# Performance work log

Hardware: AMD Instinct MI355X
Metric: run time of the kernel (lower is better)

Reference implementation:

```python
import math
import jax, jax.numpy as jnp
import numpy as np


def _proj(x, w, b):
    # 1x1x1 Conv3d == pointwise channel matmul: (B,C,T,H,W) x (O,C) -> (B,O,T,H,W)
    return jnp.einsum('bcthw,oc->bothw', x, w) + b[None, :, None, None, None]


def setup_inputs() -> dict:
    key = jax.random.key(0)
    ks = jax.random.split(key, 16)
    B, C, T, H, W = 2, 64, 16, 14, 14
    CI = C // 2
    s_in = 1.0 / math.sqrt(C)
    s_out = 1.0 / math.sqrt(CI)
    inp = {'x': jax.random.normal(ks[0], (B, C, T, H, W), jnp.float32)}
    # QKV projections for spatial (s) and temporal (t) branches: (CI, C) weights
    pnames = ['qs', 'ks', 'vs', 'qt', 'kt', 'vt']
    for i, n in enumerate(pnames):
        inp['W' + n] = jax.random.normal(ks[1 + i], (CI, C), jnp.float32) * s_in
        inp['b' + n] = jax.random.normal(ks[7 + i], (CI,), jnp.float32) * 0.01
    # output projection W: (C, CI)
    inp['Ww'] = jax.random.normal(ks[13], (C, CI), jnp.float32) * s_out
    inp['bw'] = jax.random.normal(ks[14], (C,), jnp.float32) * 0.01
    return inp


def reference(x, Wqs, bqs, Wks, bks, Wvs, bvs, Wqt, bqt, Wkt, bkt, Wvt, bvt, Ww, bw):
    B, C, T, H, W = x.shape
    CI = Wqs.shape[0]
    N = CI * H * W  # flat dim after original's raw .view (mixes channel & spatial/time)
    scale = 1.0 / math.sqrt(T)

    # ---- spatial branch: .view(B, T, -1) raw reshape of (B,CI,T,H,W) ----
    qs = _proj(x, Wqs, bqs).reshape(B, T, N).transpose(0, 2, 1)   # (B,N,T)
    ks_ = _proj(x, Wks, bks).reshape(B, T, N)                     # (B,T,N)
    vs = _proj(x, Wvs, bvs).reshape(B, T, N).transpose(0, 2, 1)   # (B,N,T)
    attn_s = jax.nn.softmax(jnp.einsum('bnt,btm->bnm', qs, ks_) * scale, axis=-1)  # (B,N,N)
    ys = jnp.einsum('bnm,bmt->bnt', attn_s, vs)                   # (B,N,T)
    ys = ys.transpose(0, 2, 1).reshape(B, CI, T, H, W)

    # ---- temporal branch: .view(B, CI*H*W, -1) raw reshape ----
    qt = _proj(x, Wqt, bqt).reshape(B, N, T).transpose(0, 2, 1)   # (B,T,N)
    kt = _proj(x, Wkt, bkt).reshape(B, N, T)                      # (B,N,T)
    vt = _proj(x, Wvt, bvt).reshape(B, N, T).transpose(0, 2, 1)   # (B,T,N)
    attn_t = jax.nn.softmax(jnp.einsum('btn,bns->bts', qt, kt) * scale, axis=-1)  # (B,T,T)
    yt = jnp.einsum('bts,bsn->btn', attn_t, vt)                   # (B,T,N)
    yt = yt.transpose(0, 2, 1).reshape(B, CI, T, H, W)

    y = ys + yt
    return _proj(y, Ww, bw) + x
```

## Files before the change

### kernel.cpp

```cpp
#include <hip/hip_runtime.h>
#include <math.h>

#define S3   3136
#define PB   100352
#define XB   200704
#define NN   6272
#define MW   7
#define MPW  896
#define TGC  49

typedef __attribute__((ext_vector_type(8))) short bf16x8;
typedef __attribute__((ext_vector_type(4))) float f32x4;

__device__ inline ushort f2bf(float f) {
    uint u = __float_as_uint(f);
    return (ushort)((u + 0x7FFFu + ((u >> 16) & 1u)) >> 16);
}

__global__ __launch_bounds__(256) void proj_kernel(
    const float* __restrict__ x,
    const float* __restrict__ W0, const float* __restrict__ b0,
    const float* __restrict__ W1, const float* __restrict__ b1,
    const float* __restrict__ W2, const float* __restrict__ b2,
    const float* __restrict__ W3, const float* __restrict__ b3,
    const float* __restrict__ W4, const float* __restrict__ b4,
    const float* __restrict__ W5, const float* __restrict__ b5,
    ushort* __restrict__ Qb, ushort* __restrict__ Kb, ushort* __restrict__ Vb,
    float* __restrict__ Qt, float* __restrict__ Kt, float* __restrict__ Vt)
{
    const float* Wp; const float* bp;
    switch (blockIdx.y) {
        case 0:  Wp = W0; bp = b0; break;
        case 1:  Wp = W1; bp = b1; break;
        case 2:  Wp = W2; bp = b2; break;
        case 3:  Wp = W3; bp = b3; break;
        case 4:  Wp = W4; bp = b4; break;
        default: Wp = W5; bp = b5; break;
    }
    int z = blockIdx.z;

    int gid = blockIdx.x * 256 + threadIdx.x;
    if (gid >= 2 * S3) return;
    int b = (gid >= S3) ? 1 : 0;
    int s = gid - b * S3;

    float xr[64];
    #pragma unroll
    for (int c = 0; c < 64; ++c) xr[c] = x[(size_t)b * XB + (size_t)c * S3 + s];

    float a[16];
    #pragma unroll
    for (int oo = 0; oo < 16; ++oo) {
        int o = z * 16 + oo;
        float acc = bp[o];
        #pragma unroll
        for (int c = 0; c < 64; ++c) acc = fmaf(Wp[o * 64 + c], xr[c], acc);
        a[oo] = acc;
    }

    if (blockIdx.y < 2) {
        const float sc = (blockIdx.y == 0) ? 0.36067376022224085f : 1.0f;
        ushort* ob = (blockIdx.y == 0) ? Qb : Kb;
        #pragma unroll
        for (int h = 0; h < 2; ++h) {
            int n = h * S3 + s;
            uint u0 = f2bf(a[0 + h] * sc)  | ((uint)f2bf(a[2 + h]  * sc) << 16);
            uint u1 = f2bf(a[4 + h] * sc)  | ((uint)f2bf(a[6 + h]  * sc) << 16);
            uint u2 = f2bf(a[8 + h] * sc)  | ((uint)f2bf(a[10 + h] * sc) << 16);
            uint u3 = f2bf(a[12 + h] * sc) | ((uint)f2bf(a[14 + h] * sc) << 16);
            *(uint4*)(ob + ((size_t)(b * NN + n) * 16 + z * 8)) = make_uint4(u0, u1, u2, u3);
        }
    } else if (blockIdx.y == 2) {
        #pragma unroll
        for (int oo = 0; oo < 16; ++oo) {
            int o = z * 16 + oo;
            Vb[(size_t)(b * 16 + (o >> 1)) * NN + (o & 1) * S3 + s] = f2bf(a[oo]);
        }
    } else {
        float* op = (blockIdx.y == 3) ? Qt : (blockIdx.y == 4) ? Kt : Vt;
        #pragma unroll
        for (int oo = 0; oo < 16; ++oo)
            op[(size_t)b * PB + (size_t)(z * 16 + oo) * S3 + s] = a[oo];
    }
}

__global__ __launch_bounds__(256) void attn_kernel(
    const ushort* __restrict__ Qb, const ushort* __restrict__ Kb,
    const ushort* __restrict__ Vb, const float* __restrict__ Qt,
    const float* __restrict__ Kt,
    float* __restrict__ Pacc, float* __restrict__ Pl, float* __restrict__ Gp)
{
    __shared__ ushort ptile[4][16 * 40];
    __shared__ float qs[128 * 16], ks[128 * 16];

    int b = blockIdx.y;

    if (blockIdx.x >= 686) {
        int c = blockIdx.x - 686;
        size_t base = (size_t)b * PB + (size_t)c * 2048;
        for (int i = threadIdx.x; i < 512; i += 256) {
            ((float4*)qs)[i] = ((const float4*)(Qt + base))[i];
            ((float4*)ks)[i] = ((const float4*)(Kt + base))[i];
        }
        __syncthreads();
        int t = threadIdx.x >> 4, s = threadIdx.x & 15;
        float acc = 0.0f;
        #pragma unroll 8
        for (int n = 0; n < 128; ++n)
            acc = fmaf(qs[n * 16 + t], ks[n * 16 + s], acc);
        Gp[(size_t)(b * TGC + c) * 256 + threadIdx.x] = acc;
        return;
    }

    int wave = __builtin_amdgcn_readfirstlane((int)(threadIdx.x >> 6));
    int lane = threadIdx.x & 63;
    int col  = lane & 15;
    int kg   = lane >> 4;
    int gw   = blockIdx.x * 4 + wave;
    int ntile = gw / 7;
    int w     = gw - ntile * 7;
    int nbase = ntile * 16;
    int m0    = w * MPW;

    bf16x8 qf = {0, 0, 0, 0, 0, 0, 0, 0};
    if (kg < 2)
        qf = *(const bf16x8*)(Qb + ((size_t)(b * NN + nbase + col) * 16 + kg * 8));

    const bf16x8 ones = {16256, 16256, 16256, 16256, 16256, 16256, 16256, 16256};
    f32x4 zero4 = {0.f, 0.f, 0.f, 0.f};
    f32x4 yacc  = zero4;
    f32x4 lacc  = zero4;

    ushort* myt = ptile[wave];

    for (int it = 0; it < MPW / 32; ++it) {
        int mb = m0 + it * 32;
        bf16x8 vf = *(const bf16x8*)(Vb + ((size_t)(b * 16 + col) * NN + mb + kg * 8));

        #pragma unroll
        for (int tile = 0; tile < 2; ++tile) {
            int mt = mb + tile * 16;
            bf16x8 kf = {0, 0, 0, 0, 0, 0, 0, 0};
            if (kg < 2)
                kf = *(const bf16x8*)(Kb + ((size_t)(b * NN + mt + col) * 16 + kg * 8));
            f32x4 st = __builtin_amdgcn_mfma_f32_16x16x32_bf16(kf, qf, zero4, 0, 0, 0);
            float p0 = __builtin_amdgcn_exp2f(st[0]);
            float p1 = __builtin_amdgcn_exp2f(st[1]);
            float p2 = __builtin_amdgcn_exp2f(st[2]);
            float p3 = __builtin_amdgcn_exp2f(st[3]);
            uint lo = f2bf(p0) | ((uint)f2bf(p1) << 16);
            uint hi = f2bf(p2) | ((uint)f2bf(p3) << 16);
            *(uint2*)(myt + (col * 40 + tile * 16 + kg * 4)) = make_uint2(lo, hi);
        }
        bf16x8 pf = *(bf16x8*)(myt + (col * 40 + kg * 8));
        yacc = __builtin_amdgcn_mfma_f32_16x16x32_bf16(vf, pf, yacc, 0, 0, 0);
        lacc = __builtin_amdgcn_mfma_f32_16x16x32_bf16(ones, pf, lacc, 0, 0, 0);
    }

    #pragma unroll
    for (int r = 0; r < 4; ++r) {
        int t = kg * 4 + r;
        Pacc[((size_t)(b * 16 + t) * MW + w) * NN + nbase + col] = yacc[r];
    }
    if (kg == 0)
        Pl[((size_t)b * MW + w) * NN + nbase + col] = lacc[0];
}

__global__ __launch_bounds__(256) void merge_final(
    const float* __restrict__ Pacc, const float* __restrict__ Pl,
    const float* __restrict__ Gp, const float* __restrict__ Vt,
    const float* __restrict__ x, const float* __restrict__ Ww,
    const float* __restrict__ bw, float* __restrict__ out)
{
    __shared__ float Lsh[256];
    __shared__ float Ash[16][17];
    __shared__ float Wsh[64 * 36];
    __shared__ float Ysh[16 * 36];

    int b  = blockIdx.y;
    int sc = blockIdx.x;

    {
        float a = 0.0f;
        for (int c = 0; c < TGC; ++c)
            a += Gp[(size_t)(b * TGC + c) * 256 + threadIdx.x];
        Lsh[threadIdx.x] = a * 0.25f;
        for (int i = threadIdx.x; i < 2048; i += 256)
            Wsh[(i >> 5) * 36 + (i & 31)] = Ww[i];
    }
    __syncthreads();
    if (threadIdx.x < 16) {
        int t = threadIdx.x;
        const float* Lr = &Lsh[t * 16];
        float mx = -1e30f;
        #pragma unroll
        for (int s = 0; s < 16; ++s) mx = fmaxf(mx, Lr[s]);
        float e[16]; float sm = 0.0f;
        #pragma unroll
        for (int s = 0; s < 16; ++s) { e[s] = __expf(Lr[s] - mx); sm += e[s]; }
        float inv = 1.0f / sm;
        #pragma unroll
        for (int s = 0; s < 16; ++s) Ash[s][t] = e[s] * inv;
    }
    __syncthreads();

    #pragma unroll
    for (int k = 0; k < 2; ++k) {
        int idx = threadIdx.x + k * 256;
        int ss = idx & 15;
        int ci = idx >> 4;
        int s  = sc * 16 + ss;
        int t  = ci >> 1;
        int nn = (ci & 1) * S3 + s;

        float a = 0.0f, l = 0.0f;
        #pragma unroll
        for (int w = 0; w < MW; ++w) {
            a += Pacc[((size_t)(b * 16 + t) * MW + w) * NN + nn];
            l += Pl[((size_t)b * MW + w) * NN + nn];
        }
        float ys = a / l;

        int t2 = nn & 15;
        const float4* vp = (const float4*)(Vt + (size_t)b * PB + (size_t)t * NN + (nn & ~15));
        float4 v0 = vp[0], v1 = vp[1], v2 = vp[2], v3 = vp[3];
        float yt = Ash[0][t2] * v0.x;
        yt = fmaf(Ash[1][t2],  v0.y, yt); yt = fmaf(Ash[2][t2],  v0.z, yt);
        yt = fmaf(Ash[3][t2],  v0.w, yt); yt = fmaf(Ash[4][t2],  v1.x, yt);
        yt = fmaf(Ash[5][t2],  v1.y, yt); yt = fmaf(Ash[6][t2],  v1.z, yt);
        yt = fmaf(Ash[7][t2],  v1.w, yt); yt = fmaf(Ash[8][t2],  v2.x, yt);
        yt = fmaf(Ash[9][t2],  v2.y, yt); yt = fmaf(Ash[10][t2], v2.z, yt);
        yt = fmaf(Ash[11][t2], v2.w, yt); yt = fmaf(Ash[12][t2], v3.x, yt);
        yt = fmaf(Ash[13][t2], v3.y, yt); yt = fmaf(Ash[14][t2], v3.z, yt);
        yt = fmaf(Ash[15][t2], v3.w, yt);

        Ysh[ss * 36 + ci] = ys + yt;
    }
    __syncthreads();

    int ss = threadIdx.x & 15;
    int cg = threadIdx.x >> 4;
    int s  = sc * 16 + ss;

    float acc[4];
    #pragma unroll
    for (int k = 0; k < 4; ++k) acc[k] = bw[cg * 4 + k];

    #pragma unroll
    for (int cb = 0; cb < 32; cb += 4) {
        float4 y4 = *(const float4*)&Ysh[ss * 36 + cb];
        #pragma unroll
        for (int k = 0; k < 4; ++k) {
            float4 w4 = *(const float4*)&Wsh[(cg * 4 + k) * 36 + cb];
            acc[k] = fmaf(w4.x, y4.x, acc[k]);
            acc[k] = fmaf(w4.y, y4.y, acc[k]);
            acc[k] = fmaf(w4.z, y4.z, acc[k]);
            acc[k] = fmaf(w4.w, y4.w, acc[k]);
        }
    }

    #pragma unroll
    for (int k = 0; k < 4; ++k) {
        int c = cg * 4 + k;
        size_t o = (size_t)b * XB + (size_t)c * S3 + s;
        out[o] = x[o] + acc[k];
    }
}

extern "C" void kernel_launch(void* const* d_in, const int* in_sizes, int n_in,
                              void* d_out, int out_size, void* d_ws, size_t ws_size,
                              hipStream_t stream)
{
    const float* x   = (const float*)d_in[0];
    const float* Wqs = (const float*)d_in[1];  const float* bqs = (const float*)d_in[2];
    const float* Wks = (const float*)d_in[3];  const float* bks = (const float*)d_in[4];
    const float* Wvs = (const float*)d_in[5];  const float* bvs = (const float*)d_in[6];
    const float* Wqt = (const float*)d_in[7];  const float* bqt = (const float*)d_in[8];
    const float* Wkt = (const float*)d_in[9];  const float* bkt = (const float*)d_in[10];
    const float* Wvt = (const float*)d_in[11]; const float* bvt = (const float*)d_in[12];
    const float* Ww  = (const float*)d_in[13]; const float* bw  = (const float*)d_in[14];

    float* ws = (float*)d_ws;
    ushort* Qb = (ushort*)(ws);
    ushort* Kb = (ushort*)(ws + 100352);
    ushort* Vb = (ushort*)(ws + 200704);
    float* Qt  = ws + 301056;
    float* Kt  = ws + 501760;
    float* Vt  = ws + 702464;
    float* Gp  = ws + 903168;
    float* Pacc = ws + 928256;
    float* Pl   = ws + 2333184;

    proj_kernel<<<dim3(25, 6, 2), 256, 0, stream>>>(
        x, Wqs, bqs, Wks, bks, Wvs, bvs, Wqt, bqt, Wkt, bkt, Wvt, bvt,
        Qb, Kb, Vb, Qt, Kt, Vt);

    attn_kernel<<<dim3(686 + TGC, 2), 256, 0, stream>>>(
        Qb, Kb, Vb, Qt, Kt, Pacc, Pl, Gp);

    merge_final<<<dim3(196, 2), 256, 0, stream>>>(
        Pacc, Pl, Gp, Vt, x, Ww, bw, (float*)d_out);
}
```

Baseline: 142.1 us.

## Fuse three kernels into one persistent kernel with grid barriers

Merges the projection, attention and merge/output kernels into one persistent launch of 512 blocks that separates the stages with software grid barriers built on atomic counters. A memset resets the counters before each launch. The projection loop now loads x in chunks of 16 channels to lower register pressure, and the attention work is spread over the waves in a grid-stride loop. This removes two kernel launch gaps, but adds barrier spin costs, a memset launch, and depends on all 512 blocks being resident at once.

```diff
diff --git a/kernel.cpp b/kernel.cpp
--- a/kernel.cpp
+++ b/kernel.cpp
@@ -8,6 +8,8 @@
 #define MW   7
 #define MPW  896
 #define TGC  49
+#define GRID 512
+#define SPB  464
 
 typedef __attribute__((ext_vector_type(8))) short bf16x8;
 typedef __attribute__((ext_vector_type(4))) float f32x4;
@@ -17,253 +19,273 @@
     return (ushort)((u + 0x7FFFu + ((u >> 16) & 1u)) >> 16);
 }
 
-__global__ __launch_bounds__(256) void proj_kernel(
-    const float* __restrict__ x,
-    const float* __restrict__ W0, const float* __restrict__ b0,
-    const float* __restrict__ W1, const float* __restrict__ b1,
-    const float* __restrict__ W2, const float* __restrict__ b2,
-    const float* __restrict__ W3, const float* __restrict__ b3,
-    const float* __restrict__ W4, const float* __restrict__ b4,
-    const float* __restrict__ W5, const float* __restrict__ b5,
-    ushort* __restrict__ Qb, ushort* __restrict__ Kb, ushort* __restrict__ Vb,
-    float* __restrict__ Qt, float* __restrict__ Kt, float* __restrict__ Vt)
+__device__ inline void grid_barrier(int* ctr, int nblk) {
+    __syncthreads();
+    if (threadIdx.x == 0) {
+        __threadfence();
+        atomicAdd(ctr, 1);
+        while (__hip_atomic_load(ctr, __ATOMIC_RELAXED,
+                                 __HIP_MEMORY_SCOPE_AGENT) < nblk)
+            __builtin_amdgcn_s_sleep(8);
+        __threadfence();
+    }
+    __syncthreads();
+}
+
+struct Params {
+    const float *x;
+    const float *W[6];
+    const float *bias[6];
+    const float *Ww, *bw;
+    int    *bar;
+    ushort *Qb, *Kb, *Vb;
+    float  *Qt, *Kt, *Vt;
+    float  *Gp, *Pacc, *Pl;
+    float  *out;
+};
+
+__global__ __launch_bounds__(256, 4) void fused_kernel(Params p)
 {
-    const float* Wp; const float* bp;
-    switch (blockIdx.y) {
-        case 0:  Wp = W0; bp = b0; break;
-        case 1:  Wp = W1; bp = b1; break;
-        case 2:  Wp = W2; bp = b2; break;
-        case 3:  Wp = W3; bp = b3; break;
-        case 4:  Wp = W4; bp = b4; break;
-        default: Wp = W5; bp = b5; break;
-    }
-    int z = blockIdx.z;
-
-    int gid = blockIdx.x * 256 + threadIdx.x;
-    if (gid >= 2 * S3) return;
-    int b = (gid >= S3) ? 1 : 0;
-    int s = gid - b * S3;
-
-    float xr[64];
-    #pragma unroll
-    for (int c = 0; c < 64; ++c) xr[c] = x[(size_t)b * XB + (size_t)c * S3 + s];
-
-    float a[16];
-    #pragma unroll
-    for (int oo = 0; oo < 16; ++oo) {
-        int o = z * 16 + oo;
-        float acc = bp[o];
+    __shared__ __align__(16) char smem[16384];
+    const int tid = threadIdx.x;
+    const int bid = blockIdx.x;
+
+    {
+        int gid = bid * 256 + tid;
+        if (gid < 75264) {
+            int bs = gid % 6272;
+            int yz = gid / 6272;
+            int y = yz >> 1, z = yz & 1;
+            int b = (bs >= S3) ? 1 : 0;
+            int s = bs - b * S3;
+
+            const float* Wp = p.W[y];
+            const float* bp = p.bias[y];
+
+            float a[16];
+            #pragma unroll
+            for (int oo = 0; oo < 16; ++oo) a[oo] = bp[z * 16 + oo];
+
+            #pragma unroll
+            for (int cc = 0; cc < 4; ++cc) {
+                float xr[16];
+                #pragma unroll
+                for (int k = 0; k < 16; ++k)
+                    xr[k] = p.x[(size_t)b * XB + (size_t)(cc * 16 + k) * S3 + s];
+                #pragma unroll
+                for (int oo = 0; oo < 16; ++oo) {
+                    int o = z * 16 + oo;
+                    #pragma unroll
+                    for (int k = 0; k < 16; ++k)
+                        a[oo] = fmaf(Wp[o * 64 + cc * 16 + k], xr[k], a[oo]);
+                }
+            }
+
+            if (y < 2) {
+                const float sc = (y == 0) ? 0.36067376022224085f : 1.0f;
+                ushort* ob = (y == 0) ? p.Qb : p.Kb;
+                #pragma unroll
+                for (int h = 0; h < 2; ++h) {
+                    int n = h * S3 + s;
+                    uint u0 = f2bf(a[0 + h] * sc)  | ((uint)f2bf(a[2 + h]  * sc) << 16);
+                    uint u1 = f2bf(a[4 + h] * sc)  | ((uint)f2bf(a[6 + h]  * sc) << 16);
+                    uint u2 = f2bf(a[8 + h] * sc)  | ((uint)f2bf(a[10 + h] * sc) << 16);
+                    uint u3 = f2bf(a[12 + h] * sc) | ((uint)f2bf(a[14 + h] * sc) << 16);
+                    *(uint4*)(ob + ((size_t)(b * NN + n) * 16 + z * 8)) =
+                        make_uint4(u0, u1, u2, u3);
+                }
+            } else if (y == 2) {
+                #pragma unroll
+                for (int oo = 0; oo < 16; ++oo) {
+                    int o = z * 16 + oo;
+                    p.Vb[(size_t)(b * 16 + (o >> 1)) * NN + (o & 1) * S3 + s] = f2bf(a[oo]);
+                }
+            } else {
+                float* op = (y == 3) ? p.Qt : (y == 4) ? p.Kt : p.Vt;
+                #pragma unroll
+                for (int oo = 0; oo < 16; ++oo)
+                    op[(size_t)b * PB + (size_t)(z * 16 + oo) * S3 + s] = a[oo];
+            }
+        }
+    }
+
+    grid_barrier(p.bar + 0, GRID);
+
+    if (bid < SPB) {
+        int wave = __builtin_amdgcn_readfirstlane((int)(tid >> 6));
+        int lane = tid & 63;
+        int col  = lane & 15;
+        int kg   = lane >> 4;
+        int gwave = bid * 4 + wave;
+        ushort* myt = (ushort*)(smem + wave * 1280);
+        const bf16x8 ones = {16256, 16256, 16256, 16256, 16256, 16256, 16256, 16256};
+        f32x4 zero4 = {0.f, 0.f, 0.f, 0.f};
+
+        for (int task = gwave; task < 2 * 2744; task += SPB * 4) {
+            int b = task / 2744;
+            int r = task - b * 2744;
+            int ntile = r / 7;
+            int w     = r - ntile * 7;
+            int nbase = ntile * 16;
+            int m0    = w * MPW;
+
+            bf16x8 qf = {0, 0, 0, 0, 0, 0, 0, 0};
+            if (kg < 2)
+                qf = *(const bf16x8*)(p.Qb + ((size_t)(b * NN + nbase + col) * 16 + kg * 8));
+
+            f32x4 yacc = zero4;
+            f32x4 lacc = zero4;
+
+            for (int it = 0; it < MPW / 32; ++it) {
+                int mb = m0 + it * 32;
+                bf16x8 vf = *(const bf16x8*)(p.Vb + ((size_t)(b * 16 + col) * NN + mb + kg * 8));
+
+                #pragma unroll
+                for (int tile = 0; tile < 2; ++tile) {
+                    int mt = mb + tile * 16;
+                    bf16x8 kf = {0, 0, 0, 0, 0, 0, 0, 0};
+                    if (kg < 2)
+                        kf = *(const bf16x8*)(p.Kb + ((size_t)(b * NN + mt + col) * 16 + kg * 8));
+                    f32x4 st = __builtin_amdgcn_mfma_f32_16x16x32_bf16(kf, qf, zero4, 0, 0, 0);
+                    float p0 = __builtin_amdgcn_exp2f(st[0]);
+                    float p1 = __builtin_amdgcn_exp2f(st[1]);
+                    float p2 = __builtin_amdgcn_exp2f(st[2]);
+                    float p3 = __builtin_amdgcn_exp2f(st[3]);
+                    uint lo = f2bf(p0) | ((uint)f2bf(p1) << 16);
+                    uint hi = f2bf(p2) | ((uint)f2bf(p3) << 16);
+                    *(uint2*)(myt + (col * 40 + tile * 16 + kg * 4)) = make_uint2(lo, hi);
+                }
+                bf16x8 pf = *(bf16x8*)(myt + (col * 40 + kg * 8));
+                yacc = __builtin_amdgcn_mfma_f32_16x16x32_bf16(vf, pf, yacc, 0, 0, 0);
+                lacc = __builtin_amdgcn_mfma_f32_16x16x32_bf16(ones, pf, lacc, 0, 0, 0);
+            }
+
+            #pragma unroll
+            for (int r4 = 0; r4 < 4; ++r4) {
+                int t = kg * 4 + r4;
+                p.Pacc[((size_t)(b * 16 + t) * MW + w) * NN + nbase + col] = yacc[r4];
+            }
+            if (kg == 0)
+                p.Pl[((size_t)b * MW + w) * NN + nbase + col] = lacc[0];
+        }
+    } else {
+        float* qs = (float*)smem;
+        float* ks = qs + 2048;
+        for (int c2 = bid - SPB; c2 < 98; c2 += GRID - SPB) {
+            int bb = c2 / TGC;
+            int ch = c2 - bb * TGC;
+            size_t base = (size_t)bb * PB + (size_t)ch * 2048;
+            __syncthreads();
+            for (int i = tid; i < 512; i += 256) {
+                ((float4*)qs)[i] = ((const float4*)(p.Qt + base))[i];
+                ((float4*)ks)[i] = ((const float4*)(p.Kt + base))[i];
+            }
+            __syncthreads();
+            int t = tid >> 4, s = tid & 15;
+            float acc = 0.0f;
+            #pragma unroll 8
+            for (int n = 0; n < 128; ++n)
+                acc = fmaf(qs[n * 16 + t], ks[n * 16 + s], acc);
+            p.Gp[(size_t)(bb * TGC + ch) * 256 + tid] = acc;
+        }
+    }
+
+    grid_barrier(p.bar + 1, GRID);
+
+    if (bid < 392) {
+        float* Lsh = (float*)smem;
+        float* Ash = Lsh + 256;
+        float* Wsh = Ash + 272;
+        float* Ysh = Wsh + 2304;
+
+        int b  = (bid >= 196) ? 1 : 0;
+        int sc = bid - b * 196;
+
+        {
+            float a = 0.0f;
+            for (int c = 0; c < TGC; ++c)
+                a += p.Gp[(size_t)(b * TGC + c) * 256 + tid];
+            Lsh[tid] = a * 0.25f;
+            for (int i = tid; i < 2048; i += 256)
+                Wsh[(i >> 5) * 36 + (i & 31)] = p.Ww[i];
+        }
+        __syncthreads();
+        if (tid < 16) {
+            int t = tid;
+            const float* Lr = &Lsh[t * 16];
+            float mx = -1e30f;
+            #pragma unroll
+            for (int s = 0; s < 16; ++s) mx = fmaxf(mx, Lr[s]);
+            float e[16]; float sm = 0.0f;
+            #pragma unroll
+            for (int s = 0; s < 16; ++s) { e[s] = __expf(Lr[s] - mx); sm += e[s]; }
+            float inv = 1.0f / sm;
+            #pragma unroll
+            for (int s = 0; s < 16; ++s) Ash[s * 17 + t] = e[s] * inv;
+        }
+        __syncthreads();
+
         #pragma unroll
-        for (int c = 0; c < 64; ++c) acc = fmaf(Wp[o * 64 + c], xr[c], acc);
-        a[oo] = acc;
-    }
-
-    if (blockIdx.y < 2) {
-        const float sc = (blockIdx.y == 0) ? 0.36067376022224085f : 1.0f;
-        ushort* ob = (blockIdx.y == 0) ? Qb : Kb;
+        for (int k = 0; k < 2; ++k) {
+            int idx = tid + k * 256;
+            int ss = idx & 15;
+            int ci = idx >> 4;
+            int s  = sc * 16 + ss;
+            int t  = ci >> 1;
+            int nn = (ci & 1) * S3 + s;
+
+            float a = 0.0f, l = 0.0f;
+            #pragma unroll
+            for (int w = 0; w < MW; ++w) {
+                a += p.Pacc[((size_t)(b * 16 + t) * MW + w) * NN + nn];
+                l += p.Pl[((size_t)b * MW + w) * NN + nn];
+            }
+            float ys = a / l;
+
+            int t2 = nn & 15;
+            const float4* vp = (const float4*)(p.Vt + (size_t)b * PB + (size_t)t * NN + (nn & ~15));
+            float4 v0 = vp[0], v1 = vp[1], v2 = vp[2], v3 = vp[3];
+            float yt = Ash[0 * 17 + t2] * v0.x;
+            yt = fmaf(Ash[1 * 17 + t2],  v0.y, yt); yt = fmaf(Ash[2 * 17 + t2],  v0.z, yt);
+            yt = fmaf(Ash[3 * 17 + t2],  v0.w, yt); yt = fmaf(Ash[4 * 17 + t2],  v1.x, yt);
+            yt = fmaf(Ash[5 * 17 + t2],  v1.y, yt); yt = fmaf(Ash[6 * 17 + t2],  v1.z, yt);
+            yt = fmaf(Ash[7 * 17 + t2],  v1.w, yt); yt = fmaf(Ash[8 * 17 + t2],  v2.x, yt);
+            yt = fmaf(Ash[9 * 17 + t2],  v2.y, yt); yt = fmaf(Ash[10 * 17 + t2], v2.z, yt);
+            yt = fmaf(Ash[11 * 17 + t2], v2.w, yt); yt = fmaf(Ash[12 * 17 + t2], v3.x, yt);
+            yt = fmaf(Ash[13 * 17 + t2], v3.y, yt); yt = fmaf(Ash[14 * 17 + t2], v3.z, yt);
+            yt = fmaf(Ash[15 * 17 + t2], v3.w, yt);
+
+            Ysh[ss * 36 + ci] = ys + yt;
+        }
+        __syncthreads();
+
+        int ss  = tid & 15;
+        int cg4 = tid >> 4;
+        int s   = sc * 16 + ss;
+
+        float acc[4];
         #pragma unroll
-        for (int h = 0; h < 2; ++h) {
-            int n = h * S3 + s;
-            uint u0 = f2bf(a[0 + h] * sc)  | ((uint)f2bf(a[2 + h]  * sc) << 16);
-            uint u1 = f2bf(a[4 + h] * sc)  | ((uint)f2bf(a[6 + h]  * sc) << 16);
-            uint u2 = f2bf(a[8 + h] * sc)  | ((uint)f2bf(a[10 + h] * sc) << 16);
-            uint u3 = f2bf(a[12 + h] * sc) | ((uint)f2bf(a[14 + h] * sc) << 16);
-            *(uint4*)(ob + ((size_t)(b * NN + n) * 16 + z * 8)) = make_uint4(u0, u1, u2, u3);
-        }
-    } else if (blockIdx.y == 2) {
+        for (int k = 0; k < 4; ++k) acc[k] = p.bw[cg4 * 4 + k];
+
         #pragma unroll
-        for (int oo = 0; oo < 16; ++oo) {
-            int o = z * 16 + oo;
-            Vb[(size_t)(b * 16 + (o >> 1)) * NN + (o & 1) * S3 + s] = f2bf(a[oo]);
-        }
-    } else {
-        float* op = (blockIdx.y == 3) ? Qt : (blockIdx.y == 4) ? Kt : Vt;
-        #pragma unroll
-        for (int oo = 0; oo < 16; ++oo)
-            op[(size_t)b * PB + (size_t)(z * 16 + oo) * S3 + s] = a[oo];
-    }
-}
-
-__global__ __launch_bounds__(256) void attn_kernel(
-    const ushort* __restrict__ Qb, const ushort* __restrict__ Kb,
-    const ushort* __restrict__ Vb, const float* __restrict__ Qt,
-    const float* __restrict__ Kt,
-    float* __restrict__ Pacc, float* __restrict__ Pl, float* __restrict__ Gp)
-{
-    __shared__ ushort ptile[4][16 * 40];
-    __shared__ float qs[128 * 16], ks[128 * 16];
-
-    int b = blockIdx.y;
-
-    if (blockIdx.x >= 686) {
-        int c = blockIdx.x - 686;
-        size_t base = (size_t)b * PB + (size_t)c * 2048;
-        for (int i = threadIdx.x; i < 512; i += 256) {
-            ((float4*)qs)[i] = ((const float4*)(Qt + base))[i];
-            ((float4*)ks)[i] = ((const float4*)(Kt + base))[i];
-        }
-        __syncthreads();
-        int t = threadIdx.x >> 4, s = threadIdx.x & 15;
-        float acc = 0.0f;
-        #pragma unroll 8
-        for (int n = 0; n < 128; ++n)
-            acc = fmaf(qs[n * 16 + t], ks[n * 16 + s], acc);
-        Gp[(size_t)(b * TGC + c) * 256 + threadIdx.x] = acc;
-        return;
-    }
-
-    int wave = __builtin_amdgcn_readfirstlane((int)(threadIdx.x >> 6));
-    int lane = threadIdx.x & 63;
-    int col  = lane & 15;
-    int kg   = lane >> 4;
-    int gw   = blockIdx.x * 4 + wave;
-    int ntile = gw / 7;
-    int w     = gw - ntile * 7;
-    int nbase = ntile * 16;
-    int m0    = w * MPW;
-
-    bf16x8 qf = {0, 0, 0, 0, 0, 0, 0, 0};
-    if (kg < 2)
-        qf = *(const bf16x8*)(Qb + ((size_t)(b * NN + nbase + col) * 16 + kg * 8));
-
-    const bf16x8 ones = {16256, 16256, 16256, 16256, 16256, 16256, 16256, 16256};
-    f32x4 zero4 = {0.f, 0.f, 0.f, 0.f};
-    f32x4 yacc  = zero4;
-    f32x4 lacc  = zero4;
-
-    ushort* myt = ptile[wave];
-
-    for (int it = 0; it < MPW / 32; ++it) {
-        int mb = m0 + it * 32;
-        bf16x8 vf = *(const bf16x8*)(Vb + ((size_t)(b * 16 + col) * NN + mb + kg * 8));
-
-        #pragma unroll
-        for (int tile = 0; tile < 2; ++tile) {
-            int mt = mb + tile * 16;
-            bf16x8 kf = {0, 0, 0, 0, 0, 0, 0, 0};
-            if (kg < 2)
-                kf = *(const bf16x8*)(Kb + ((size_t)(b * NN + mt + col) * 16 + kg * 8));
-            f32x4 st = __builtin_amdgcn_mfma_f32_16x16x32_bf16(kf, qf, zero4, 0, 0, 0);
-            float p0 = __builtin_amdgcn_exp2f(st[0]);
-            float p1 = __builtin_amdgcn_exp2f(st[1]);
-            float p2 = __builtin_amdgcn_exp2f(st[2]);
-            float p3 = __builtin_amdgcn_exp2f(st[3]);
-            uint lo = f2bf(p0) | ((uint)f2bf(p1) << 16);
-            uint hi = f2bf(p2) | ((uint)f2bf(p3) << 16);
-            *(uint2*)(myt + (col * 40 + tile * 16 + kg * 4)) = make_uint2(lo, hi);
-        }
-        bf16x8 pf = *(bf16x8*)(myt + (col * 40 + kg * 8));
-        yacc = __builtin_amdgcn_mfma_f32_16x16x32_bf16(vf, pf, yacc, 0, 0, 0);
-        lacc = __builtin_amdgcn_mfma_f32_16x16x32_bf16(ones, pf, lacc, 0, 0, 0);
-    }
-
-    #pragma unroll
-    for (int r = 0; r < 4; ++r) {
-        int t = kg * 4 + r;
-        Pacc[((size_t)(b * 16 + t) * MW + w) * NN + nbase + col] = yacc[r];
-    }
-    if (kg == 0)
-        Pl[((size_t)b * MW + w) * NN + nbase + col] = lacc[0];
-}
-
-__global__ __launch_bounds__(256) void merge_final(
-    const float* __restrict__ Pacc, const float* __restrict__ Pl,
-    const float* __restrict__ Gp, const float* __restrict__ Vt,
-    const float* __restrict__ x, const float* __restrict__ Ww,
-    const float* __restrict__ bw, float* __restrict__ out)
-{
-    __shared__ float Lsh[256];
-    __shared__ float Ash[16][17];
-    __shared__ float Wsh[64 * 36];
-    __shared__ float Ysh[16 * 36];
-
-    int b  = blockIdx.y;
-    int sc = blockIdx.x;
-
-    {
-        float a = 0.0f;
-        for (int c = 0; c < TGC; ++c)
-            a += Gp[(size_t)(b * TGC + c) * 256 + threadIdx.x];
-        Lsh[threadIdx.x] = a * 0.25f;
-        for (int i = threadIdx.x; i < 2048; i += 256)
-            Wsh[(i >> 5) * 36 + (i & 31)] = Ww[i];
-    }
-    __syncthreads();
-    if (threadIdx.x < 16) {
-        int t = threadIdx.x;
-        const float* Lr = &Lsh[t * 16];
-        float mx = -1e30f;
-        #pragma unroll
-        for (int s = 0; s < 16; ++s) mx = fmaxf(mx, Lr[s]);
-        float e[16]; float sm = 0.0f;
-        #pragma unroll
-        for (int s = 0; s < 16; ++s) { e[s] = __expf(Lr[s] - mx); sm += e[s]; }
-        float inv = 1.0f / sm;
-        #pragma unroll
-        for (int s = 0; s < 16; ++s) Ash[s][t] = e[s] * inv;
-    }
-    __syncthreads();
-
-    #pragma unroll
-    for (int k = 0; k < 2; ++k) {
-        int idx = threadIdx.x + k * 256;
-        int ss = idx & 15;
-        int ci = idx >> 4;
-        int s  = sc * 16 + ss;
-        int t  = ci >> 1;
-        int nn = (ci & 1) * S3 + s;
-
-        float a = 0.0f, l = 0.0f;
-        #pragma unroll
-        for (int w = 0; w < MW; ++w) {
-            a += Pacc[((size_t)(b * 16 + t) * MW + w) * NN + nn];
-            l += Pl[((size_t)b * MW + w) * NN + nn];
-        }
-        float ys = a / l;
-
-        int t2 = nn & 15;
-        const float4* vp = (const float4*)(Vt + (size_t)b * PB + (size_t)t * NN + (nn & ~15));
-        float4 v0 = vp[0], v1 = vp[1], v2 = vp[2], v3 = vp[3];
-        float yt = Ash[0][t2] * v0.x;
-        yt = fmaf(Ash[1][t2],  v0.y, yt); yt = fmaf(Ash[2][t2],  v0.z, yt);
-        yt = fmaf(Ash[3][t2],  v0.w, yt); yt = fmaf(Ash[4][t2],  v1.x, yt);
-        yt = fmaf(Ash[5][t2],  v1.y, yt); yt = fmaf(Ash[6][t2],  v1.z, yt);
-        yt = fmaf(Ash[7][t2],  v1.w, yt); yt = fmaf(Ash[8][t2],  v2.x, yt);
-        yt = fmaf(Ash[9][t2],  v2.y, yt); yt = fmaf(Ash[10][t2], v2.z, yt);
-        yt = fmaf(Ash[11][t2], v2.w, yt); yt = fmaf(Ash[12][t2], v3.x, yt);
-        yt = fmaf(Ash[13][t2], v3.y, yt); yt = fmaf(Ash[14][t2], v3.z, yt);
-        yt = fmaf(Ash[15][t2], v3.w, yt);
-
-        Ysh[ss * 36 + ci] = ys + yt;
-    }
-    __syncthreads();
-
-    int ss = threadIdx.x & 15;
-    int cg = threadIdx.x >> 4;
-    int s  = sc * 16 + ss;
-
-    float acc[4];
-    #pragma unroll
-    for (int k = 0; k < 4; ++k) acc[k] = bw[cg * 4 + k];
-
-    #pragma unroll
-    for (int cb = 0; cb < 32; cb += 4) {
-        float4 y4 = *(const float4*)&Ysh[ss * 36 + cb];
+        for (int cb = 0; cb < 32; cb += 4) {
+            float4 y4 = *(const float4*)&Ysh[ss * 36 + cb];
+            #pragma unroll
+            for (int k = 0; k < 4; ++k) {
+                float4 w4 = *(const float4*)&Wsh[(cg4 * 4 + k) * 36 + cb];
+                acc[k] = fmaf(w4.x, y4.x, acc[k]);
+                acc[k] = fmaf(w4.y, y4.y, acc[k]);
+                acc[k] = fmaf(w4.z, y4.z, acc[k]);
+                acc[k] = fmaf(w4.w, y4.w, acc[k]);
+            }
+        }
+
         #pragma unroll
         for (int k = 0; k < 4; ++k) {
-            float4 w4 = *(const float4*)&Wsh[(cg * 4 + k) * 36 + cb];
-            acc[k] = fmaf(w4.x, y4.x, acc[k]);
-            acc[k] = fmaf(w4.y, y4.y, acc[k]);
-            acc[k] = fmaf(w4.z, y4.z, acc[k]);
-            acc[k] = fmaf(w4.w, y4.w, acc[k]);
-        }
-    }
-
-    #pragma unroll
-    for (int k = 0; k < 4; ++k) {
-        int c = cg * 4 + k;
-        size_t o = (size_t)b * XB + (size_t)c * S3 + s;
-        out[o] = x[o] + acc[k];
+            int c = cg4 * 4 + k;
+            size_t o = (size_t)b * XB + (size_t)c * S3 + s;
+            p.out[o] = p.x[o] + acc[k];
+        }
     }
 }
 
@@ -271,33 +293,28 @@
                               void* d_out, int out_size, void* d_ws, size_t ws_size,
                               hipStream_t stream)
 {
-    const float* x   = (const float*)d_in[0];
-    const float* Wqs = (const float*)d_in[1];  const float* bqs = (const float*)d_in[2];
-    const float* Wks = (const float*)d_in[3];  const float* bks = (const float*)d_in[4];
-    const float* Wvs = (const float*)d_in[5];  const float* bvs = (const float*)d_in[6];
-    const float* Wqt = (const float*)d_in[7];  const float* bqt = (const float*)d_in[8];
-    const float* Wkt = (const float*)d_in[9];  const float* bkt = (const float*)d_in[10];
-    const float* Wvt = (const float*)d_in[11]; const float* bvt = (const float*)d_in[12];
-    const float* Ww  = (const float*)d_in[13]; const float* bw  = (const float*)d_in[14];
+    Params p;
+    p.x = (const float*)d_in[0];
+    for (int i = 0; i < 6; ++i) {
+        p.W[i]    = (const float*)d_in[1 + 2 * i];
+        p.bias[i] = (const float*)d_in[2 + 2 * i];
+    }
+    p.Ww = (const float*)d_in[13];
+    p.bw = (const float*)d_in[14];
 
     float* ws = (float*)d_ws;
-    ushort* Qb = (ushort*)(ws);
-    ushort* Kb = (ushort*)(ws + 100352);
-    ushort* Vb = (ushort*)(ws + 200704);
-    float* Qt  = ws + 301056;
-    float* Kt  = ws + 501760;
-    float* Vt  = ws + 702464;
-    float* Gp  = ws + 903168;
-    float* Pacc = ws + 928256;
-    float* Pl   = ws + 2333184;
-
-    proj_kernel<<<dim3(25, 6, 2), 256, 0, stream>>>(
-        x, Wqs, bqs, Wks, bks, Wvs, bvs, Wqt, bqt, Wkt, bkt, Wvt, bvt,
-        Qb, Kb, Vb, Qt, Kt, Vt);
-
-    attn_kernel<<<dim3(686 + TGC, 2), 256, 0, stream>>>(
-        Qb, Kb, Vb, Qt, Kt, Pacc, Pl, Gp);
-
-    merge_final<<<dim3(196, 2), 256, 0, stream>>>(
-        Pacc, Pl, Gp, Vt, x, Ww, bw, (float*)d_out);
+    p.bar = (int*)ws;
+    p.Qb  = (ushort*)(ws + 4);
+    p.Kb  = (ushort*)(ws + 100356);
+    p.Vb  = (ushort*)(ws + 200708);
+    p.Qt  = ws + 301060;
+    p.Kt  = ws + 501764;
+    p.Vt  = ws + 702468;
+    p.Gp  = ws + 903172;
+    p.Pacc = ws + 928260;
+    p.Pl   = ws + 2333188;
+    p.out  = (float*)d_out;
+
+    hipMemsetAsync(p.bar, 0, 2 * sizeof(int), stream);
+    fused_kernel<<<GRID, 256, 0, stream>>>(p);
 }
```

Result: slower. 279.9 us (+97.0%).

## Reduce spatial attention partials in-block and finalize temporal softmax via atomic counter

Applied to the files above, without the earlier changes.

The spatial attention now gives each block one 16-row tile, with its four waves splitting the key range. The waves combine their partial numerators and denominators in shared memory and write the normalized output directly, so the 7-way Pacc/Pl partial buffers in global memory are no longer needed. The temporal Gram computation uses fewer, larger chunks, and the last block to finish (tracked by an atomic counter reset in proj_kernel) computes the 16x16 softmax once per batch. merge_final then only reads finished Y and attention values. This removes a large amount of intermediate global traffic and redundant per-block softmax work, at the cost of fewer blocks (less parallelism), a longer per-wave loop, and reliance on fence and atomic ordering.

```diff
diff --git a/kernel.cpp b/kernel.cpp
--- a/kernel.cpp
+++ b/kernel.cpp
@@ -5,9 +5,6 @@
 #define PB   100352
 #define XB   200704
 #define NN   6272
-#define MW   7
-#define MPW  896
-#define TGC  49
 
 typedef __attribute__((ext_vector_type(8))) short bf16x8;
 typedef __attribute__((ext_vector_type(4))) float f32x4;
@@ -26,8 +23,12 @@
     const float* __restrict__ W4, const float* __restrict__ b4,
     const float* __restrict__ W5, const float* __restrict__ b5,
     ushort* __restrict__ Qb, ushort* __restrict__ Kb, ushort* __restrict__ Vb,
-    float* __restrict__ Qt, float* __restrict__ Kt, float* __restrict__ Vt)
+    float* __restrict__ Qt, float* __restrict__ Kt, float* __restrict__ Vt,
+    int* __restrict__ cnt)
 {
+    if (blockIdx.x == 0 && blockIdx.y == 0 && blockIdx.z == 0 && threadIdx.x < 2)
+        cnt[threadIdx.x] = 0;
+
     const float* Wp; const float* bp;
     switch (blockIdx.y) {
         case 0:  Wp = W0; bp = b0; break;
@@ -84,174 +85,199 @@
     }
 }
 
-__global__ __launch_bounds__(256) void attn_kernel(
+__global__ __launch_bounds__(256, 4) void attn_kernel(
     const ushort* __restrict__ Qb, const ushort* __restrict__ Kb,
     const ushort* __restrict__ Vb, const float* __restrict__ Qt,
     const float* __restrict__ Kt,
-    float* __restrict__ Pacc, float* __restrict__ Pl, float* __restrict__ Gp)
+    float* __restrict__ Y, float* __restrict__ Gpart,
+    float* __restrict__ At, int* __restrict__ cnt)
 {
-    __shared__ ushort ptile[4][16 * 40];
-    __shared__ float qs[128 * 16], ks[128 * 16];
-
-    int b = blockIdx.y;
-
-    if (blockIdx.x >= 686) {
-        int c = blockIdx.x - 686;
-        size_t base = (size_t)b * PB + (size_t)c * 2048;
-        for (int i = threadIdx.x; i < 512; i += 256) {
-            ((float4*)qs)[i] = ((const float4*)(Qt + base))[i];
-            ((float4*)ks)[i] = ((const float4*)(Kt + base))[i];
-        }
+    __shared__ __align__(16) char smem[16384];
+    const int tid = threadIdx.x;
+    const int bid = blockIdx.x;
+
+    if (bid < 784) {
+        ushort* ptile = (ushort*)smem;
+        float*  smY   = (float*)(smem + 5120);
+        float*  sml   = (float*)(smem + 9472);
+
+        int wave = __builtin_amdgcn_readfirstlane((int)(tid >> 6));
+        int lane = tid & 63;
+        int col  = lane & 15;
+        int kg   = lane >> 4;
+        int b    = (bid >= 392) ? 1 : 0;
+        int ntile = bid - b * 392;
+        int nbase = ntile * 16;
+        int m0    = wave * 1568;
+
+        bf16x8 qf = {0, 0, 0, 0, 0, 0, 0, 0};
+        if (kg < 2)
+            qf = *(const bf16x8*)(Qb + ((size_t)(b * NN + nbase + col) * 16 + kg * 8));
+
+        const bf16x8 ones = {16256, 16256, 16256, 16256, 16256, 16256, 16256, 16256};
+        f32x4 zero4 = {0.f, 0.f, 0.f, 0.f};
+        f32x4 yacc  = zero4;
+        f32x4 lacc  = zero4;
+
+        ushort* myt = ptile + wave * 640;
+
+        for (int it = 0; it < 49; ++it) {
+            int mb = m0 + it * 32;
+            bf16x8 vf = *(const bf16x8*)(Vb + ((size_t)(b * 16 + col) * NN + mb + kg * 8));
+
+            #pragma unroll
+            for (int tile = 0; tile < 2; ++tile) {
+                int mt = mb + tile * 16;
+                bf16x8 kf = {0, 0, 0, 0, 0, 0, 0, 0};
+                if (kg < 2)
+                    kf = *(const bf16x8*)(Kb + ((size_t)(b * NN + mt + col) * 16 + kg * 8));
+                f32x4 st = __builtin_amdgcn_mfma_f32_16x16x32_bf16(kf, qf, zero4, 0, 0, 0);
+                float p0 = __builtin_amdgcn_exp2f(st[0]);
+                float p1 = __builtin_amdgcn_exp2f(st[1]);
+                float p2 = __builtin_amdgcn_exp2f(st[2]);
+                float p3 = __builtin_amdgcn_exp2f(st[3]);
+                uint lo = f2bf(p0) | ((uint)f2bf(p1) << 16);
+                uint hi = f2bf(p2) | ((uint)f2bf(p3) << 16);
+                *(uint2*)(myt + (col * 40 + tile * 16 + kg * 4)) = make_uint2(lo, hi);
+            }
+            bf16x8 pf = *(bf16x8*)(myt + (col * 40 + kg * 8));
+            yacc = __builtin_amdgcn_mfma_f32_16x16x32_bf16(vf, pf, yacc, 0, 0, 0);
+            lacc = __builtin_amdgcn_mfma_f32_16x16x32_bf16(ones, pf, lacc, 0, 0, 0);
+        }
+
+        #pragma unroll
+        for (int r = 0; r < 4; ++r)
+            smY[(wave * 16 + kg * 4 + r) * 17 + col] = yacc[r];
+        if (kg == 0) sml[wave * 16 + col] = lacc[0];
         __syncthreads();
-        int t = threadIdx.x >> 4, s = threadIdx.x & 15;
+
+        int t  = tid >> 4;
+        int nn = tid & 15;
+        float a = smY[(0 * 16 + t) * 17 + nn] + smY[(1 * 16 + t) * 17 + nn]
+                + smY[(2 * 16 + t) * 17 + nn] + smY[(3 * 16 + t) * 17 + nn];
+        float l = sml[0 * 16 + nn] + sml[1 * 16 + nn]
+                + sml[2 * 16 + nn] + sml[3 * 16 + nn];
+        Y[(size_t)b * PB + (size_t)t * NN + nbase + nn] = a / l;
+    } else {
+        float* qs = (float*)smem;
+        float* ks = qs + 1568;
+        int*   flag = (int*)(smem + 16000);
+
+        int gb = bid - 784;
+        int b  = gb >> 4;
+        int ch = gb & 15;
+        int t  = tid >> 4, s2 = tid & 15;
+
         float acc = 0.0f;
-        #pragma unroll 8
-        for (int n = 0; n < 128; ++n)
-            acc = fmaf(qs[n * 16 + t], ks[n * 16 + s], acc);
-        Gp[(size_t)(b * TGC + c) * 256 + threadIdx.x] = acc;
-        return;
-    }
-
-    int wave = __builtin_amdgcn_readfirstlane((int)(threadIdx.x >> 6));
-    int lane = threadIdx.x & 63;
-    int col  = lane & 15;
-    int kg   = lane >> 4;
-    int gw   = blockIdx.x * 4 + wave;
-    int ntile = gw / 7;
-    int w     = gw - ntile * 7;
-    int nbase = ntile * 16;
-    int m0    = w * MPW;
-
-    bf16x8 qf = {0, 0, 0, 0, 0, 0, 0, 0};
-    if (kg < 2)
-        qf = *(const bf16x8*)(Qb + ((size_t)(b * NN + nbase + col) * 16 + kg * 8));
-
-    const bf16x8 ones = {16256, 16256, 16256, 16256, 16256, 16256, 16256, 16256};
-    f32x4 zero4 = {0.f, 0.f, 0.f, 0.f};
-    f32x4 yacc  = zero4;
-    f32x4 lacc  = zero4;
-
-    ushort* myt = ptile[wave];
-
-    for (int it = 0; it < MPW / 32; ++it) {
-        int mb = m0 + it * 32;
-        bf16x8 vf = *(const bf16x8*)(Vb + ((size_t)(b * 16 + col) * NN + mb + kg * 8));
-
-        #pragma unroll
-        for (int tile = 0; tile < 2; ++tile) {
-            int mt = mb + tile * 16;
-            bf16x8 kf = {0, 0, 0, 0, 0, 0, 0, 0};
-            if (kg < 2)
-                kf = *(const bf16x8*)(Kb + ((size_t)(b * NN + mt + col) * 16 + kg * 8));
-            f32x4 st = __builtin_amdgcn_mfma_f32_16x16x32_bf16(kf, qf, zero4, 0, 0, 0);
-            float p0 = __builtin_amdgcn_exp2f(st[0]);
-            float p1 = __builtin_amdgcn_exp2f(st[1]);
-            float p2 = __builtin_amdgcn_exp2f(st[2]);
-            float p3 = __builtin_amdgcn_exp2f(st[3]);
-            uint lo = f2bf(p0) | ((uint)f2bf(p1) << 16);
-            uint hi = f2bf(p2) | ((uint)f2bf(p3) << 16);
-            *(uint2*)(myt + (col * 40 + tile * 16 + kg * 4)) = make_uint2(lo, hi);
-        }
-        bf16x8 pf = *(bf16x8*)(myt + (col * 40 + kg * 8));
-        yacc = __builtin_amdgcn_mfma_f32_16x16x32_bf16(vf, pf, yacc, 0, 0, 0);
-        lacc = __builtin_amdgcn_mfma_f32_16x16x32_bf16(ones, pf, lacc, 0, 0, 0);
-    }
-
-    #pragma unroll
-    for (int r = 0; r < 4; ++r) {
-        int t = kg * 4 + r;
-        Pacc[((size_t)(b * 16 + t) * MW + w) * NN + nbase + col] = yacc[r];
-    }
-    if (kg == 0)
-        Pl[((size_t)b * MW + w) * NN + nbase + col] = lacc[0];
+        for (int sub = 0; sub < 4; ++sub) {
+            size_t base = (size_t)b * PB + (size_t)(ch * 392 + sub * 98) * 16;
+            __syncthreads();
+            for (int i = tid; i < 392; i += 256) {
+                ((float4*)qs)[i] = ((const float4*)(Qt + base))[i];
+                ((float4*)ks)[i] = ((const float4*)(Kt + base))[i];
+            }
+            __syncthreads();
+            #pragma unroll 7
+            for (int n = 0; n < 98; ++n)
+                acc = fmaf(qs[n * 16 + t], ks[n * 16 + s2], acc);
+        }
+        Gpart[(size_t)(b * 16 + ch) * 256 + tid] = acc;
+
+        __threadfence();
+        __syncthreads();
+        if (tid == 0) {
+            int old = atomicAdd(cnt + b, 1);
+            *flag = (old == 15);
+        }
+        __syncthreads();
+        if (*flag) {
+            __threadfence();
+            float a = 0.0f;
+            #pragma unroll
+            for (int c = 0; c < 16; ++c)
+                a += Gpart[(size_t)(b * 16 + c) * 256 + tid];
+            qs[tid] = a * 0.25f;
+            __syncthreads();
+            if (tid < 16) {
+                const float* Lr = &qs[tid * 16];
+                float mx = -1e30f;
+                #pragma unroll
+                for (int s = 0; s < 16; ++s) mx = fmaxf(mx, Lr[s]);
+                float e[16]; float sm = 0.0f;
+                #pragma unroll
+                for (int s = 0; s < 16; ++s) { e[s] = __expf(Lr[s] - mx); sm += e[s]; }
+                float inv = 1.0f / sm;
+                #pragma unroll
+                for (int s = 0; s < 16; ++s) At[b * 256 + tid * 16 + s] = e[s] * inv;
+            }
+        }
+    }
 }
 
 __global__ __launch_bounds__(256) void merge_final(
-    const float* __restrict__ Pacc, const float* __restrict__ Pl,
-    const float* __restrict__ Gp, const float* __restrict__ Vt,
-    const float* __restrict__ x, const float* __restrict__ Ww,
-    const float* __restrict__ bw, float* __restrict__ out)
+    const float* __restrict__ Y, const float* __restrict__ At,
+    const float* __restrict__ Vt, const float* __restrict__ x,
+    const float* __restrict__ Ww, const float* __restrict__ bw,
+    float* __restrict__ out)
 {
-    __shared__ float Lsh[256];
-    __shared__ float Ash[16][17];
+    __shared__ float Ash[16 * 17];
     __shared__ float Wsh[64 * 36];
     __shared__ float Ysh[16 * 36];
 
     int b  = blockIdx.y;
     int sc = blockIdx.x;
+    int tid = threadIdx.x;
 
     {
-        float a = 0.0f;
-        for (int c = 0; c < TGC; ++c)
-            a += Gp[(size_t)(b * TGC + c) * 256 + threadIdx.x];
-        Lsh[threadIdx.x] = a * 0.25f;
-        for (int i = threadIdx.x; i < 2048; i += 256)
+        int s2 = tid >> 4, t2 = tid & 15;
+        Ash[s2 * 17 + t2] = At[b * 256 + t2 * 16 + s2];
+        for (int i = tid; i < 2048; i += 256)
             Wsh[(i >> 5) * 36 + (i & 31)] = Ww[i];
     }
     __syncthreads();
-    if (threadIdx.x < 16) {
-        int t = threadIdx.x;
-        const float* Lr = &Lsh[t * 16];
-        float mx = -1e30f;
-        #pragma unroll
-        for (int s = 0; s < 16; ++s) mx = fmaxf(mx, Lr[s]);
-        float e[16]; float sm = 0.0f;
-        #pragma unroll
-        for (int s = 0; s < 16; ++s) { e[s] = __expf(Lr[s] - mx); sm += e[s]; }
-        float inv = 1.0f / sm;
-        #pragma unroll
-        for (int s = 0; s < 16; ++s) Ash[s][t] = e[s] * inv;
-    }
-    __syncthreads();
 
     #pragma unroll
     for (int k = 0; k < 2; ++k) {
-        int idx = threadIdx.x + k * 256;
+        int idx = tid + k * 256;
         int ss = idx & 15;
         int ci = idx >> 4;
         int s  = sc * 16 + ss;
         int t  = ci >> 1;
         int nn = (ci & 1) * S3 + s;
 
-        float a = 0.0f, l = 0.0f;
-        #pragma unroll
-        for (int w = 0; w < MW; ++w) {
-            a += Pacc[((size_t)(b * 16 + t) * MW + w) * NN + nn];
-            l += Pl[((size_t)b * MW + w) * NN + nn];
-        }
-        float ys = a / l;
+        float ys = Y[(size_t)b * PB + (size_t)ci * S3 + s];
 
         int t2 = nn & 15;
         const float4* vp = (const float4*)(Vt + (size_t)b * PB + (size_t)t * NN + (nn & ~15));
         float4 v0 = vp[0], v1 = vp[1], v2 = vp[2], v3 = vp[3];
-        float yt = Ash[0][t2] * v0.x;
-        yt = fmaf(Ash[1][t2],  v0.y, yt); yt = fmaf(Ash[2][t2],  v0.z, yt);
-        yt = fmaf(Ash[3][t2],  v0.w, yt); yt = fmaf(Ash[4][t2],  v1.x, yt);
-        yt = fmaf(Ash[5][t2],  v1.y, yt); yt = fmaf(Ash[6][t2],  v1.z, yt);
-        yt = fmaf(Ash[7][t2],  v1.w, yt); yt = fmaf(Ash[8][t2],  v2.x, yt);
-        yt = fmaf(Ash[9][t2],  v2.y, yt); yt = fmaf(Ash[10][t2], v2.z, yt);
-        yt = fmaf(Ash[11][t2], v2.w, yt); yt = fmaf(Ash[12][t2], v3.x, yt);
-        yt = fmaf(Ash[13][t2], v3.y, yt); yt = fmaf(Ash[14][t2], v3.z, yt);
-        yt = fmaf(Ash[15][t2], v3.w, yt);
+        float yt = Ash[0 * 17 + t2] * v0.x;
+        yt = fmaf(Ash[1 * 17 + t2],  v0.y, yt); yt = fmaf(Ash[2 * 17 + t2],  v0.z, yt);
+        yt = fmaf(Ash[3 * 17 + t2],  v0.w, yt); yt = fmaf(Ash[4 * 17 + t2],  v1.x, yt);
+        yt = fmaf(Ash[5 * 17 + t2],  v1.y, yt); yt = fmaf(Ash[6 * 17 + t2],  v1.z, yt);
+        yt = fmaf(Ash[7 * 17 + t2],  v1.w, yt); yt = fmaf(Ash[8 * 17 + t2],  v2.x, yt);
+        yt = fmaf(Ash[9 * 17 + t2],  v2.y, yt); yt = fmaf(Ash[10 * 17 + t2], v2.z, yt);
+        yt = fmaf(Ash[11 * 17 + t2], v2.w, yt); yt = fmaf(Ash[12 * 17 + t2], v3.x, yt);
+        yt = fmaf(Ash[13 * 17 + t2], v3.y, yt); yt = fmaf(Ash[14 * 17 + t2], v3.z, yt);
+        yt = fmaf(Ash[15 * 17 + t2], v3.w, yt);
 
         Ysh[ss * 36 + ci] = ys + yt;
     }
     __syncthreads();
 
-    int ss = threadIdx.x & 15;
-    int cg = threadIdx.x >> 4;
-    int s  = sc * 16 + ss;
+    int ss  = tid & 15;
+    int cg4 = tid >> 4;
+    int s   = sc * 16 + ss;
 
     float acc[4];
     #pragma unroll
-    for (int k = 0; k < 4; ++k) acc[k] = bw[cg * 4 + k];
+    for (int k = 0; k < 4; ++k) acc[k] = bw[k * 16 + cg4];
 
     #pragma unroll
     for (int cb = 0; cb < 32; cb += 4) {
         float4 y4 = *(const float4*)&Ysh[ss * 36 + cb];
         #pragma unroll
         for (int k = 0; k < 4; ++k) {
-            float4 w4 = *(const float4*)&Wsh[(cg * 4 + k) * 36 + cb];
+            float4 w4 = *(const float4*)&Wsh[(k * 16 + cg4) * 36 + cb];
             acc[k] = fmaf(w4.x, y4.x, acc[k]);
             acc[k] = fmaf(w4.y, y4.y, acc[k]);
             acc[k] = fmaf(w4.z, y4.z, acc[k]);
@@ -261,7 +287,7 @@
 
     #pragma unroll
     for (int k = 0; k < 4; ++k) {
-        int c = cg * 4 + k;
+        int c = k * 16 + cg4;
         size_t o = (size_t)b * XB + (size_t)c * S3 + s;
         out[o] = x[o] + acc[k];
     }
@@ -281,23 +307,23 @@
     const float* Ww  = (const float*)d_in[13]; const float* bw  = (const float*)d_in[14];
 
     float* ws = (float*)d_ws;
-    ushort* Qb = (ushort*)(ws);
-    ushort* Kb = (ushort*)(ws + 100352);
-    ushort* Vb = (ushort*)(ws + 200704);
-    float* Qt  = ws + 301056;
-    float* Kt  = ws + 501760;
-    float* Vt  = ws + 702464;
-    float* Gp  = ws + 903168;
-    float* Pacc = ws + 928256;
-    float* Pl   = ws + 2333184;
+    int*    cnt = (int*)ws;
+    ushort* Qb  = (ushort*)(ws + 4);
+    ushort* Kb  = (ushort*)(ws + 100356);
+    ushort* Vb  = (ushort*)(ws + 200708);
+    float* Qt   = ws + 301060;
+    float* Kt   = ws + 501764;
+    float* Vt   = ws + 702468;
+    float* Y    = ws + 903172;
+    float* Gpart = ws + 1103876;
+    float* At    = ws + 1112068;
 
     proj_kernel<<<dim3(25, 6, 2), 256, 0, stream>>>(
         x, Wqs, bqs, Wks, bks, Wvs, bvs, Wqt, bqt, Wkt, bkt, Wvt, bvt,
-        Qb, Kb, Vb, Qt, Kt, Vt);
-
-    attn_kernel<<<dim3(686 + TGC, 2), 256, 0, stream>>>(
-        Qb, Kb, Vb, Qt, Kt, Pacc, Pl, Gp);
+        Qb, Kb, Vb, Qt, Kt, Vt, cnt);
+
+    attn_kernel<<<816, 256, 0, stream>>>(Qb, Kb, Vb, Qt, Kt, Y, Gpart, At, cnt);
 
     merge_final<<<dim3(196, 2), 256, 0, stream>>>(
-        Pacc, Pl, Gp, Vt, x, Ww, bw, (float*)d_out);
-}
+        Y, At, Vt, x, Ww, bw, (float*)d_out);
+}
```

Measured after the change: 149.8 us. +5.5%, slower.
